# Kernel optimization log

Hardware: AMD Instinct MI355X
Metric: run time of the kernel (lower is better)

Reference implementation:

```python
import jax, jax.numpy as jnp
import numpy as np

B, T, H, DK = 4, 2048, 16, 64
F = H * DK
CK, NL = 64, 16  # chunk_size, num left chunks
MIN_VAL = float(np.finfo(np.float16).min)


def chunk_mask(size, ck, nl):
    # row i attends cols [max((i//ck - nl)*ck, 0), (i//ck + 1)*ck)
    i = jnp.arange(size)
    start = jnp.maximum((i // ck - nl) * ck, 0)
    end = (i // ck + 1) * ck
    j = jnp.arange(size)
    return (j[None, :] >= start[:, None]) & (j[None, :] < end[:, None])


def setup_inputs() -> dict:
    rng = jax.random.key(0)
    ks = jax.random.split(rng, 14)
    s = 1.0 / np.sqrt(F)
    mask = jnp.broadcast_to(chunk_mask(T, CK, NL)[None], (B, T, T))  # padding mask all-True & chunk band
    return {
        "query": jax.random.normal(ks[0], (B, T, F), jnp.float32),
        "key": jax.random.normal(ks[1], (B, T, F), jnp.float32),
        "value": jax.random.normal(ks[2], (B, T, F), jnp.float32),
        "pos_emb": jax.random.normal(ks[3], (1, T, F), jnp.float32),
        "mask": mask,
        "Wq": jax.random.normal(ks[4], (F, F), jnp.float32) * s,
        "bq": jnp.zeros((F,), jnp.float32),
        "Wk": jax.random.normal(ks[5], (F, F), jnp.float32) * s,
        "bk": jnp.zeros((F,), jnp.float32),
        "Wv": jax.random.normal(ks[6], (F, F), jnp.float32) * s,
        "bv": jnp.zeros((F,), jnp.float32),
        "Wp": jax.random.normal(ks[7], (F, F), jnp.float32) * s,
        "Wo": jax.random.normal(ks[8], (F, F), jnp.float32) * s,
        "bo": jnp.zeros((F,), jnp.float32),
        "pos_bias_u": jax.random.normal(ks[9], (H, DK), jnp.float32) * 0.05,
        "pos_bias_v": jax.random.normal(ks[10], (H, DK), jnp.float32) * 0.05,
    }


def reference(query, key, value, pos_emb, mask, Wq, bq, Wk, bk, Wv, bv, Wp, Wo, bo, pos_bias_u, pos_bias_v):
    b, t1, _ = query.shape
    t2 = key.shape[1]
    q = (query @ Wq.T + bq).reshape(b, t1, H, DK)            # (b, t1, h, d)
    k = (key @ Wk.T + bk).reshape(b, t2, H, DK).transpose(0, 2, 1, 3)   # (b, h, t2, d)
    v = (value @ Wv.T + bv).reshape(b, t2, H, DK).transpose(0, 2, 1, 3)  # (b, h, t2, d)
    p = (pos_emb @ Wp.T).reshape(pos_emb.shape[0], -1, H, DK).transpose(0, 2, 1, 3)[0]  # (h, t2, d)
    # matrix_ac: content score with bias u; matrix_bd: position score with bias v (no rel_shift in forward)
    matrix_ac = jnp.einsum('bthd,bhsd->bhts', q + pos_bias_u, k)
    matrix_bd = jnp.einsum('bthd,hsd->bhts', q + pos_bias_v, p)
    scores = (matrix_ac + matrix_bd) / np.sqrt(DK)
    m = mask[:, None, :, :]                                   # (b, 1, t1, t2)
    scores = jnp.where(m, scores, MIN_VAL)
    attn = jax.nn.softmax(scores, axis=-1)
    attn = jnp.where(m, attn, 0.0)
    x = jnp.einsum('bhts,bhsd->bthd', attn, v).reshape(b, t1, F)
    return x @ Wo.T + bo
```

## Files before the change

kernel.cpp:

```cpp
#include <hip/hip_runtime.h>
#include <hip/hip_bf16.h>

#define B_ 4
#define T_ 2048
#define H_ 16
#define DK_ 64
#define F_ 1024
#define SCALE_LOG2 0.18033688011112042f

typedef __bf16 bf16x8 __attribute__((ext_vector_type(8)));
typedef __bf16 bf16x4 __attribute__((ext_vector_type(4)));
typedef float f32x4 __attribute__((ext_vector_type(4)));

__device__ __forceinline__ void async_cp16(const void* g, void* l) {
  __builtin_amdgcn_global_load_lds((const __attribute__((address_space(1))) void*)g,
                                   (__attribute__((address_space(3))) void*)l, 16, 0, 0);
}

struct CvtArgs {
  const float* src[9];
  __bf16* dst[9];
  int n[9];
};
__global__ void cvt_all(CvtArgs a) {
  int t = blockIdx.y;
  int i = (blockIdx.x * 256 + threadIdx.x) * 8;
  if (i >= a.n[t]) return;
  const float* in = a.src[t];
  __bf16* out = a.dst[t];
  float4 x = *(const float4*)(in + i);
  float4 y = *(const float4*)(in + i + 4);
  bf16x8 o;
  o[0] = (__bf16)x.x; o[1] = (__bf16)x.y; o[2] = (__bf16)x.z; o[3] = (__bf16)x.w;
  o[4] = (__bf16)y.x; o[5] = (__bf16)y.y; o[6] = (__bf16)y.z; o[7] = (__bf16)y.w;
  *(bf16x8*)(out + i) = o;
}

struct GemmQKVP {
  const __bf16* W[4];
  const __bf16* Act[4];
  const float* bias[4];
  __bf16* out[4];
  int Nblocks[4];
};
__global__ __launch_bounds__(256) void gemm_qkvp(GemmQKVP g) {
  const int z = blockIdx.z;
  if ((int)blockIdx.x >= g.Nblocks[z]) return;
  const __bf16* __restrict__ A = g.W[z];
  const __bf16* __restrict__ Bm = g.Act[z];
  const float* __restrict__ bias = g.bias[z];
  __bf16* __restrict__ Cout = g.out[z];
  constexpr int K = F_;
  __shared__ __bf16 As[128 * 32];
  __shared__ __bf16 Bs[128 * 32];
  const int tid = threadIdx.x;
  const int wave = tid >> 6, lane = tid & 63;
  const int mrow = lane & 15, quad = lane >> 4;
  const long m0 = (long)blockIdx.y * 128;
  const long n0 = (long)blockIdx.x * 128;
  const int wr = (wave >> 1) * 64, wc = (wave & 1) * 64;
  const int srow = lane >> 2;
  const int scol = (lane & 3) * 8;
  f32x4 acc[4][4] = {};
  for (int k0 = 0; k0 < K; k0 += 32) {
    if (k0) __syncthreads();
    for (int ph = 0; ph < 2; ++ph) {
      int rb = ph * 64 + wave * 16;
      async_cp16(A + (m0 + rb + srow) * (long)K + k0 + scol, As + rb * 32);
      async_cp16(Bm + (n0 + rb + srow) * (long)K + k0 + scol, Bs + rb * 32);
    }
    __syncthreads();
    bf16x8 af[4], bf[4];
    for (int i = 0; i < 4; i++) af[i] = *(const bf16x8*)&As[(wr + i * 16 + mrow) * 32 + quad * 8];
    for (int j = 0; j < 4; j++) bf[j] = *(const bf16x8*)&Bs[(wc + j * 16 + mrow) * 32 + quad * 8];
    for (int i = 0; i < 4; i++)
      for (int j = 0; j < 4; j++)
        acc[i][j] = __builtin_amdgcn_mfma_f32_16x16x32_bf16(af[i], bf[j], acc[i][j], 0, 0, 0);
  }
  for (int i = 0; i < 4; i++) {
    int frow = (int)m0 + wr + i * 16 + quad * 4;
    float4 b4 = bias ? *(const float4*)&bias[frow] : make_float4(0.f, 0.f, 0.f, 0.f);
    int h = frow >> 6, dbase = frow & 63;
    for (int j = 0; j < 4; j++) {
      int token = (int)n0 + wc + j * 16 + mrow;
      int bb = token >> 11, tt = token & 2047;
      bf16x4 pk;
      pk[0] = (__bf16)(acc[i][j][0] + b4.x);
      pk[1] = (__bf16)(acc[i][j][1] + b4.y);
      pk[2] = (__bf16)(acc[i][j][2] + b4.z);
      pk[3] = (__bf16)(acc[i][j][3] + b4.w);
      *(bf16x4*)&Cout[(((long)(bb * H_ + h)) * T_ + tt) * DK_ + dbase] = pk;
    }
  }
}

__global__ __launch_bounds__(256) void gemm_out(
    const __bf16* __restrict__ A, const __bf16* __restrict__ Bm,
    float* __restrict__ Cout, const float* __restrict__ bias, int N, int K) {
  __shared__ __bf16 As[128 * 32];
  __shared__ __bf16 Bs[128 * 32];
  const int tid = threadIdx.x;
  const int wave = tid >> 6, lane = tid & 63;
  const int mrow = lane & 15, quad = lane >> 4;
  const long m0 = (long)blockIdx.y * 128, n0 = (long)blockIdx.x * 128;
  const int wr = (wave >> 1) * 64, wc = (wave & 1) * 64;
  const int srow = lane >> 2;
  const int scol = (lane & 3) * 8;
  f32x4 acc[4][4] = {};
  for (int k0 = 0; k0 < K; k0 += 32) {
    if (k0) __syncthreads();
    for (int ph = 0; ph < 2; ++ph) {
      int rb = ph * 64 + wave * 16;
      async_cp16(A + (m0 + rb + srow) * (long)K + k0 + scol, As + rb * 32);
      async_cp16(Bm + (n0 + rb + srow) * (long)K + k0 + scol, Bs + rb * 32);
    }
    __syncthreads();
    bf16x8 af[4], bf[4];
    for (int i = 0; i < 4; i++) af[i] = *(const bf16x8*)&As[(wr + i * 16 + mrow) * 32 + quad * 8];
    for (int j = 0; j < 4; j++) bf[j] = *(const bf16x8*)&Bs[(wc + j * 16 + mrow) * 32 + quad * 8];
    for (int i = 0; i < 4; i++)
      for (int j = 0; j < 4; j++)
        acc[i][j] = __builtin_amdgcn_mfma_f32_16x16x32_bf16(af[i], bf[j], acc[i][j], 0, 0, 0);
  }
  for (int i = 0; i < 4; i++) {
    int row = (int)m0 + wr + i * 16 + quad * 4;
    for (int j = 0; j < 4; j++) {
      int col = (int)n0 + wc + j * 16 + mrow;
      float bval = bias[col];
      for (int r = 0; r < 4; r++)
        Cout[(long)(row + r) * N + col] = acc[i][j][r] + bval;
    }
  }
}

__global__ __launch_bounds__(256) void prep(
    const __bf16* __restrict__ Ph, __bf16* __restrict__ Kh,
    const __bf16* __restrict__ Vh, __bf16* __restrict__ Vth,
    const float* __restrict__ u, const float* __restrict__ vb,
    float* __restrict__ biasC) {
  __shared__ __bf16 Vl[64 * 72];
  const int tc = blockIdx.x, h = blockIdx.y, b = blockIdx.z;
  const int tid = threadIdx.x;
  const int r4 = tid >> 2, c16 = (tid & 3) * 16;
  const long bh = b * H_ + h;
  const long kbase = (bh * T_ + tc * 64 + r4) * DK_ + c16;
  const long pbase = (((long)h) * T_ + tc * 64 + r4) * DK_ + c16;
  bf16x8 k0 = *(const bf16x8*)&Kh[kbase];
  bf16x8 k1 = *(const bf16x8*)&Kh[kbase + 8];
  bf16x8 p0 = *(const bf16x8*)&Ph[pbase];
  bf16x8 p1 = *(const bf16x8*)&Ph[pbase + 8];
  float4 u0 = *(const float4*)&u[h * 64 + c16];
  float4 u1 = *(const float4*)&u[h * 64 + c16 + 4];
  float4 u2 = *(const float4*)&u[h * 64 + c16 + 8];
  float4 u3 = *(const float4*)&u[h * 64 + c16 + 12];
  float4 v0 = *(const float4*)&vb[h * 64 + c16];
  float4 v1 = *(const float4*)&vb[h * 64 + c16 + 4];
  float4 v2 = *(const float4*)&vb[h * 64 + c16 + 8];
  float4 v3 = *(const float4*)&vb[h * 64 + c16 + 12];
  float s = 0.f;
  {
    const float uu[16] = {u0.x,u0.y,u0.z,u0.w,u1.x,u1.y,u1.z,u1.w,u2.x,u2.y,u2.z,u2.w,u3.x,u3.y,u3.z,u3.w};
    const float vv[16] = {v0.x,v0.y,v0.z,v0.w,v1.x,v1.y,v1.z,v1.w,v2.x,v2.y,v2.z,v2.w,v3.x,v3.y,v3.z,v3.w};
#pragma unroll
    for (int j = 0; j < 8; j++) {
      s += (float)k0[j] * uu[j] + (float)p0[j] * vv[j];
      s += (float)k1[j] * uu[8 + j] + (float)p1[j] * vv[8 + j];
    }
  }
  bf16x8 kp0, kp1;
#pragma unroll
  for (int j = 0; j < 8; j++) {
    kp0[j] = (__bf16)((float)k0[j] + (float)p0[j]);
    kp1[j] = (__bf16)((float)k1[j] + (float)p1[j]);
  }
  *(bf16x8*)&Kh[kbase] = kp0;
  *(bf16x8*)&Kh[kbase + 8] = kp1;
  s += __shfl_xor(s, 1);
  s += __shfl_xor(s, 2);
  if ((tid & 3) == 0) biasC[bh * T_ + tc * 64 + r4] = s * SCALE_LOG2;
  const long vbase = (bh * T_ + tc * 64 + r4) * DK_ + c16;
  bf16x8 vv0 = *(const bf16x8*)&Vh[vbase];
  bf16x8 vv1 = *(const bf16x8*)&Vh[vbase + 8];
  *(bf16x8*)&Vl[r4 * 72 + c16] = vv0;
  *(bf16x8*)&Vl[r4 * 72 + c16 + 8] = vv1;
  __syncthreads();
  const int d4 = tid >> 2, tcol = (tid & 3) * 16;
  bf16x8 o0, o1;
#pragma unroll
  for (int j = 0; j < 8; j++) {
    o0[j] = Vl[(tcol + j) * 72 + d4];
    o1[j] = Vl[(tcol + 8 + j) * 72 + d4];
  }
  long obase = (bh * DK_ + d4) * T_ + tc * 64 + tcol;
  *(bf16x8*)&Vth[obase] = o0;
  *(bf16x8*)&Vth[obase + 8] = o1;
}

template <int FULL>
__device__ __forceinline__ void attn_step2(
    int s0, long bh, int tid, int wave, int mrow, int quad,
    const __bf16* __restrict__ Kh, const __bf16* __restrict__ Vth,
    const float* __restrict__ Bp, const bf16x8 (&qf)[4][2],
    __bf16* Pl, __bf16* Vt, f32x4 accO[4], f32x4& accL) {
  __syncthreads();
  if (FULL) {
#pragma unroll
    for (int p = 0; p < 4; ++p) {
      int idx = tid + p * 256;
      int row = idx >> 4, colg = (idx & 15) * 8;
      *(bf16x8*)&Vt[row * 136 + colg] =
          *(const bf16x8*)&Vth[(bh * DK_ + row) * T_ + s0 + colg];
    }
  } else {
#pragma unroll
    for (int p = 0; p < 2; ++p) {
      int idx = tid + p * 256;
      int row = idx >> 3, colg = (idx & 7) * 8;
      *(bf16x8*)&Vt[row * 136 + colg] =
          *(const bf16x8*)&Vth[(bh * DK_ + row) * T_ + s0 + colg];
    }
  }
  if (FULL || wave < 2) {
    const int krow = s0 + wave * 32;
    bf16x8 kf[2][2];
#pragma unroll
    for (int nt = 0; nt < 2; ++nt)
#pragma unroll
      for (int kh = 0; kh < 2; ++kh)
        kf[nt][kh] = *(const bf16x8*)&Kh[(bh * T_ + krow + nt * 16 + mrow) * DK_ + kh * 32 + quad * 8];
    float bias01[2] = {Bp[krow + mrow], Bp[krow + 16 + mrow]};
    f32x4 s[4][2];
#pragma unroll
    for (int mt = 0; mt < 4; ++mt)
#pragma unroll
      for (int nt = 0; nt < 2; ++nt) {
        f32x4 a = {0.f, 0.f, 0.f, 0.f};
        a = __builtin_amdgcn_mfma_f32_16x16x32_bf16(qf[mt][0], kf[nt][0], a, 0, 0, 0);
        a = __builtin_amdgcn_mfma_f32_16x16x32_bf16(qf[mt][1], kf[nt][1], a, 0, 0, 0);
        s[mt][nt] = a;
      }
#pragma unroll
    for (int mt = 0; mt < 4; ++mt)
#pragma unroll
      for (int nt = 0; nt < 2; ++nt)
#pragma unroll
        for (int r = 0; r < 4; ++r) {
          float p = __builtin_amdgcn_exp2f(s[mt][nt][r] * SCALE_LOG2 + bias01[nt]);
          Pl[(mt * 16 + quad * 4 + r) * 136 + wave * 32 + nt * 16 + mrow] = (__bf16)p;
        }
  }
  __syncthreads();
  constexpr int NKT = FULL ? 4 : 2;
  bf16x8 ones;
#pragma unroll
  for (int j = 0; j < 8; ++j) ones[j] = (__bf16)1.0f;
  bf16x8 ap[NKT];
#pragma unroll
  for (int kt = 0; kt < NKT; ++kt)
    ap[kt] = *(const bf16x8*)&Pl[(wave * 16 + mrow) * 136 + kt * 32 + quad * 8];
#pragma unroll
  for (int kt = 0; kt < NKT; ++kt) {
    accL = __builtin_amdgcn_mfma_f32_16x16x32_bf16(ap[kt], ones, accL, 0, 0, 0);
#pragma unroll
    for (int nt = 0; nt < 4; ++nt) {
      bf16x8 bv = *(const bf16x8*)&Vt[(nt * 16 + mrow) * 136 + kt * 32 + quad * 8];
      accO[nt] = __builtin_amdgcn_mfma_f32_16x16x32_bf16(ap[kt], bv, accO[nt], 0, 0, 0);
    }
  }
}

__global__ __launch_bounds__(256) void attn_banded(
    const __bf16* __restrict__ Qh, const __bf16* __restrict__ Kh,
    const __bf16* __restrict__ Vth, const float* __restrict__ biasC,
    __bf16* __restrict__ X) {
  __shared__ __bf16 Pl[64 * 136];
  __shared__ __bf16 Vt[64 * 136];
  const int qc = blockIdx.x, h = blockIdx.y, b = blockIdx.z;
  const int tid = threadIdx.x, wave = tid >> 6, lane = tid & 63;
  const int mrow = lane & 15, quad = lane >> 4;
  const long bh = b * H_ + h;
  const int span = (qc >= 16 ? 17 : qc + 1);
  const int s_lo = (qc + 1 - span) * 64, s_hi = (qc + 1) * 64;
  const float* Bp = biasC + bh * T_;
  bf16x8 qf[4][2];
#pragma unroll
  for (int mt = 0; mt < 4; ++mt)
#pragma unroll
    for (int kh = 0; kh < 2; ++kh)
      qf[mt][kh] = *(const bf16x8*)&Qh[(bh * T_ + qc * 64 + mt * 16 + mrow) * DK_ + kh * 32 + quad * 8];
  f32x4 accO[4] = {};
  f32x4 accL = {0.f, 0.f, 0.f, 0.f};
  int s0 = s_lo;
  if (span & 1) {
    attn_step2<0>(s0, bh, tid, wave, mrow, quad, Kh, Vth, Bp, qf, Pl, Vt, accO, accL);
    s0 += 64;
  }
  for (; s0 < s_hi; s0 += 128)
    attn_step2<1>(s0, bh, tid, wave, mrow, quad, Kh, Vth, Bp, qf, Pl, Vt, accO, accL);
#pragma unroll
  for (int r = 0; r < 4; ++r) {
    float inv = 1.0f / accL[r];
    int t = qc * 64 + wave * 16 + quad * 4 + r;
#pragma unroll
    for (int nt = 0; nt < 4; ++nt)
      X[((long)(b * T_ + t) * H_ + h) * DK_ + nt * 16 + mrow] = (__bf16)(accO[nt][r] * inv);
  }
}

extern "C" void kernel_launch(void* const* d_in, const int* in_sizes, int n_in,
                              void* d_out, int out_size, void* d_ws, size_t ws_size,
                              hipStream_t stream) {
  (void)in_sizes; (void)n_in; (void)out_size; (void)ws_size;
  const float* query = (const float*)d_in[0];
  const float* key   = (const float*)d_in[1];
  const float* value = (const float*)d_in[2];
  const float* pos   = (const float*)d_in[3];
  const float* Wq = (const float*)d_in[5];
  const float* bq = (const float*)d_in[6];
  const float* Wk = (const float*)d_in[7];
  const float* bk = (const float*)d_in[8];
  const float* Wv = (const float*)d_in[9];
  const float* bv = (const float*)d_in[10];
  const float* Wp = (const float*)d_in[11];
  const float* Wo = (const float*)d_in[12];
  const float* bo = (const float*)d_in[13];
  const float* pu = (const float*)d_in[14];
  const float* pvb = (const float*)d_in[15];

  const long NQ = (long)B_ * T_ * F_;
  const long NP = (long)T_ * F_;
  const long NW = (long)F_ * F_;
  char* ws = (char*)d_ws;
  __bf16* qb  = (__bf16*)ws; ws += NQ * 2;
  __bf16* kb  = (__bf16*)ws; ws += NQ * 2;
  __bf16* vbm = (__bf16*)ws; ws += NQ * 2;
  __bf16* pb  = (__bf16*)ws; ws += NP * 2;
  __bf16* wqb = (__bf16*)ws; ws += NW * 2;
  __bf16* wkb = (__bf16*)ws; ws += NW * 2;
  __bf16* wvb = (__bf16*)ws; ws += NW * 2;
  __bf16* wpb = (__bf16*)ws; ws += NW * 2;
  __bf16* wob = (__bf16*)ws; ws += NW * 2;
  __bf16* Qh  = (__bf16*)ws; ws += NQ * 2;
  __bf16* Kh  = (__bf16*)ws; ws += NQ * 2;
  __bf16* Vh  = (__bf16*)ws; ws += NQ * 2;
  __bf16* Ph  = (__bf16*)ws; ws += NP * 2;
  float*  biasC = (float*)ws; ws += (long)B_ * H_ * T_ * 4;
  __bf16* Vth = kb;
  __bf16* Xb  = qb;

  {
    CvtArgs ca;
    ca.src[0] = query; ca.dst[0] = qb;  ca.n[0] = (int)NQ;
    ca.src[1] = key;   ca.dst[1] = kb;  ca.n[1] = (int)NQ;
    ca.src[2] = value; ca.dst[2] = vbm; ca.n[2] = (int)NQ;
    ca.src[3] = pos;   ca.dst[3] = pb;  ca.n[3] = (int)NP;
    ca.src[4] = Wq;    ca.dst[4] = wqb; ca.n[4] = (int)NW;
    ca.src[5] = Wk;    ca.dst[5] = wkb; ca.n[5] = (int)NW;
    ca.src[6] = Wv;    ca.dst[6] = wvb; ca.n[6] = (int)NW;
    ca.src[7] = Wp;    ca.dst[7] = wpb; ca.n[7] = (int)NW;
    ca.src[8] = Wo;    ca.dst[8] = wob; ca.n[8] = (int)NW;
    cvt_all<<<dim3(4096, 9), 256, 0, stream>>>(ca);
  }
  {
    GemmQKVP g;
    g.W[0] = wqb; g.Act[0] = qb;  g.bias[0] = bq;      g.out[0] = Qh; g.Nblocks[0] = 64;
    g.W[1] = wkb; g.Act[1] = kb;  g.bias[1] = bk;      g.out[1] = Kh; g.Nblocks[1] = 64;
    g.W[2] = wvb; g.Act[2] = vbm; g.bias[2] = bv;      g.out[2] = Vh; g.Nblocks[2] = 64;
    g.W[3] = wpb; g.Act[3] = pb;  g.bias[3] = nullptr; g.out[3] = Ph; g.Nblocks[3] = 16;
    gemm_qkvp<<<dim3(64, 8, 4), 256, 0, stream>>>(g);
  }
  prep<<<dim3(32, 16, 4), 256, 0, stream>>>(Ph, Kh, Vh, Vth, pu, pvb, biasC);
  attn_banded<<<dim3(32, 16, 4), 256, 0, stream>>>(Qh, Kh, Vth, biasC, Xb);
  gemm_out<<<dim3(8, 64), 256, 0, stream>>>(Xb, wob, (float*)d_out, bo, F_, F_);
}
```

Before: 421.3 us.

## Rewrite QKVP projection GEMM as 256x256 double-buffered 8-wave pipelined kernel

Replaces the 128x128, 4-wave QKVP projection GEMM with a 256x256 tile, 512-thread kernel. It uses a 128KB double-buffered LDS ring with XOR-swizzled layout and asynchronous global-to-LDS loads interleaved between four MFMA phases, managed with explicit vmcnt waits, barriers and setprio. The goal is to hide global latency, avoid LDS bank conflicts and raise arithmetic intensity per loaded byte. The cost is fewer blocks (512 total) and heavy register and LDS use, so occupancy and tail effects could hurt, especially for the small P projection.

Result: faster. 404.0 us (-4.1%).

```diff
diff --git a/kernel.cpp b/kernel.cpp
--- a/kernel.cpp
+++ b/kernel.cpp
@@ -36,60 +36,153 @@
   *(bf16x8*)(out + i) = o;
 }
 
-struct GemmQKVP {
-  const __bf16* W[4];
-  const __bf16* Act[4];
+struct G8 {
+  const __bf16* A[4];
+  const __bf16* Bm[4];
   const float* bias[4];
   __bf16* out[4];
-  int Nblocks[4];
+  int nx[4];
 };
-__global__ __launch_bounds__(256) void gemm_qkvp(GemmQKVP g) {
+
+__global__ __launch_bounds__(512, 2) void gemm_qkvp8(G8 g) {
   const int z = blockIdx.z;
-  if ((int)blockIdx.x >= g.Nblocks[z]) return;
-  const __bf16* __restrict__ A = g.W[z];
-  const __bf16* __restrict__ Bm = g.Act[z];
+  if ((int)blockIdx.x >= g.nx[z]) return;
+  constexpr int K = F_;
+  constexpr int NT = K / 64;
+  __shared__ __bf16 LDS[65536];
+  const __bf16* __restrict__ A = g.A[z];
+  const __bf16* __restrict__ Bmm = g.Bm[z];
   const float* __restrict__ bias = g.bias[z];
-  __bf16* __restrict__ Cout = g.out[z];
-  constexpr int K = F_;
-  __shared__ __bf16 As[128 * 32];
-  __shared__ __bf16 Bs[128 * 32];
+  __bf16* __restrict__ Co = g.out[z];
   const int tid = threadIdx.x;
   const int wave = tid >> 6, lane = tid & 63;
   const int mrow = lane & 15, quad = lane >> 4;
-  const long m0 = (long)blockIdx.y * 128;
-  const long n0 = (long)blockIdx.x * 128;
-  const int wr = (wave >> 1) * 64, wc = (wave & 1) * 64;
-  const int srow = lane >> 2;
-  const int scol = (lane & 3) * 8;
-  f32x4 acc[4][4] = {};
-  for (int k0 = 0; k0 < K; k0 += 32) {
-    if (k0) __syncthreads();
-    for (int ph = 0; ph < 2; ++ph) {
-      int rb = ph * 64 + wave * 16;
-      async_cp16(A + (m0 + rb + srow) * (long)K + k0 + scol, As + rb * 32);
-      async_cp16(Bm + (n0 + rb + srow) * (long)K + k0 + scol, Bs + rb * 32);
-    }
-    __syncthreads();
-    bf16x8 af[4], bf[4];
-    for (int i = 0; i < 4; i++) af[i] = *(const bf16x8*)&As[(wr + i * 16 + mrow) * 32 + quad * 8];
-    for (int j = 0; j < 4; j++) bf[j] = *(const bf16x8*)&Bs[(wc + j * 16 + mrow) * 32 + quad * 8];
-    for (int i = 0; i < 4; i++)
-      for (int j = 0; j < 4; j++)
-        acc[i][j] = __builtin_amdgcn_mfma_f32_16x16x32_bf16(af[i], bf[j], acc[i][j], 0, 0, 0);
-  }
-  for (int i = 0; i < 4; i++) {
-    int frow = (int)m0 + wr + i * 16 + quad * 4;
+  const int wm = wave >> 2, wn = wave & 3;
+  const long m0 = (long)blockIdx.y * 256;
+  const long n0 = (long)blockIdx.x * 256;
+  const int srow = tid >> 3;
+  const int sslot = tid & 7;
+  const int scol = ((sslot ^ (srow & 7)) * 8);
+  const __bf16* sA = A + (m0 + srow) * K + scol;
+  const __bf16* sB = Bmm + (n0 + srow) * K + scol;
+  const int ldsw = wave * 512;
+  const int csw0 = ((quad) ^ (mrow & 7)) * 8;
+  const int csw1 = ((4 + quad) ^ (mrow & 7)) * 8;
+
+#define STAGE_A(t_, h_)                                              \
+  do {                                                               \
+    __bf16* lb_ = &LDS[(((t_)&1) * 2 + (h_)) * 8192 + ldsw];         \
+    const __bf16* ga_ = sA + (h_) * (128 * K) + (t_)*64;             \
+    async_cp16(ga_, lb_);                                            \
+    async_cp16(ga_ + 64 * K, lb_ + 4096);                            \
+  } while (0)
+#define STAGE_B(t_, h_)                                              \
+  do {                                                               \
+    __bf16* lb_ = &LDS[32768 + (((t_)&1) * 2 + (h_)) * 8192 + ldsw]; \
+    const __bf16* gb_ = sB + (h_) * (128 * K) + (t_)*64;             \
+    async_cp16(gb_, lb_);                                            \
+    async_cp16(gb_ + 64 * K, lb_ + 4096);                            \
+  } while (0)
+
+  f32x4 acc[8][4] = {};
+  bf16x8 af[8][2], bf[4][2];
+  STAGE_A(0, 0); STAGE_A(0, 1); STAGE_B(0, 0); STAGE_B(0, 1);
+  STAGE_A(1, 0); STAGE_A(1, 1);
+
+#pragma unroll 2
+  for (int t = 0; t < NT; ++t) {
+    const int d = t & 1;
+    const __bf16* Ab = &LDS[(d * 2 + wm) * 8192];
+    const __bf16* Bb = &LDS[32768 + (d * 2 + (wn >> 1)) * 8192 + (wn & 1) * 4096];
+    if (t + 1 < NT) {
+      STAGE_B(t + 1, 0);
+      asm volatile("s_waitcnt vmcnt(6)" ::: "memory");
+    } else {
+      asm volatile("s_waitcnt vmcnt(0)" ::: "memory");
+    }
+    __builtin_amdgcn_s_barrier();
+#pragma unroll
+    for (int fr = 0; fr < 4; ++fr) {
+      af[fr][0] = *(const bf16x8*)&Ab[(fr * 16 + mrow) * 64 + csw0];
+      af[fr][1] = *(const bf16x8*)&Ab[(fr * 16 + mrow) * 64 + csw1];
+    }
+#pragma unroll
+    for (int fc = 0; fc < 2; ++fc) {
+      bf[fc][0] = *(const bf16x8*)&Bb[(fc * 16 + mrow) * 64 + csw0];
+      bf[fc][1] = *(const bf16x8*)&Bb[(fc * 16 + mrow) * 64 + csw1];
+    }
+    __builtin_amdgcn_s_setprio(1);
+#pragma unroll
+    for (int fr = 0; fr < 4; ++fr)
+#pragma unroll
+      for (int fc = 0; fc < 2; ++fc) {
+        acc[fr][fc] = __builtin_amdgcn_mfma_f32_16x16x32_bf16(af[fr][0], bf[fc][0], acc[fr][fc], 0, 0, 0);
+        acc[fr][fc] = __builtin_amdgcn_mfma_f32_16x16x32_bf16(af[fr][1], bf[fc][1], acc[fr][fc], 0, 0, 0);
+      }
+    __builtin_amdgcn_s_setprio(0);
+    __builtin_amdgcn_s_barrier();
+    if (t + 1 < NT) STAGE_B(t + 1, 1);
+#pragma unroll
+    for (int fr = 4; fr < 8; ++fr) {
+      af[fr][0] = *(const bf16x8*)&Ab[(fr * 16 + mrow) * 64 + csw0];
+      af[fr][1] = *(const bf16x8*)&Ab[(fr * 16 + mrow) * 64 + csw1];
+    }
+#pragma unroll
+    for (int fc = 2; fc < 4; ++fc) {
+      bf[fc][0] = *(const bf16x8*)&Bb[(fc * 16 + mrow) * 64 + csw0];
+      bf[fc][1] = *(const bf16x8*)&Bb[(fc * 16 + mrow) * 64 + csw1];
+    }
+    __builtin_amdgcn_s_setprio(1);
+#pragma unroll
+    for (int fr = 4; fr < 8; ++fr)
+#pragma unroll
+      for (int fc = 2; fc < 4; ++fc) {
+        acc[fr][fc] = __builtin_amdgcn_mfma_f32_16x16x32_bf16(af[fr][0], bf[fc][0], acc[fr][fc], 0, 0, 0);
+        acc[fr][fc] = __builtin_amdgcn_mfma_f32_16x16x32_bf16(af[fr][1], bf[fc][1], acc[fr][fc], 0, 0, 0);
+      }
+    __builtin_amdgcn_s_setprio(0);
+    __builtin_amdgcn_s_barrier();
+    if (t + 2 < NT) STAGE_A(t + 2, 0);
+    __builtin_amdgcn_s_setprio(1);
+#pragma unroll
+    for (int fr = 0; fr < 4; ++fr)
+#pragma unroll
+      for (int fc = 2; fc < 4; ++fc) {
+        acc[fr][fc] = __builtin_amdgcn_mfma_f32_16x16x32_bf16(af[fr][0], bf[fc][0], acc[fr][fc], 0, 0, 0);
+        acc[fr][fc] = __builtin_amdgcn_mfma_f32_16x16x32_bf16(af[fr][1], bf[fc][1], acc[fr][fc], 0, 0, 0);
+      }
+    __builtin_amdgcn_s_setprio(0);
+    __builtin_amdgcn_s_barrier();
+    if (t + 2 < NT) STAGE_A(t + 2, 1);
+    __builtin_amdgcn_s_setprio(1);
+#pragma unroll
+    for (int fr = 4; fr < 8; ++fr)
+#pragma unroll
+      for (int fc = 0; fc < 2; ++fc) {
+        acc[fr][fc] = __builtin_amdgcn_mfma_f32_16x16x32_bf16(af[fr][0], bf[fc][0], acc[fr][fc], 0, 0, 0);
+        acc[fr][fc] = __builtin_amdgcn_mfma_f32_16x16x32_bf16(af[fr][1], bf[fc][1], acc[fr][fc], 0, 0, 0);
+      }
+    __builtin_amdgcn_s_setprio(0);
+    __builtin_amdgcn_s_barrier();
+  }
+#undef STAGE_A
+#undef STAGE_B
+
+#pragma unroll
+  for (int fr = 0; fr < 8; ++fr) {
+    int frow = (int)m0 + wm * 128 + fr * 16 + quad * 4;
     float4 b4 = bias ? *(const float4*)&bias[frow] : make_float4(0.f, 0.f, 0.f, 0.f);
     int h = frow >> 6, dbase = frow & 63;
-    for (int j = 0; j < 4; j++) {
-      int token = (int)n0 + wc + j * 16 + mrow;
+#pragma unroll
+    for (int fc = 0; fc < 4; ++fc) {
+      int token = (int)n0 + wn * 64 + fc * 16 + mrow;
       int bb = token >> 11, tt = token & 2047;
       bf16x4 pk;
-      pk[0] = (__bf16)(acc[i][j][0] + b4.x);
-      pk[1] = (__bf16)(acc[i][j][1] + b4.y);
-      pk[2] = (__bf16)(acc[i][j][2] + b4.z);
-      pk[3] = (__bf16)(acc[i][j][3] + b4.w);
-      *(bf16x4*)&Cout[(((long)(bb * H_ + h)) * T_ + tt) * DK_ + dbase] = pk;
+      pk[0] = (__bf16)(acc[fr][fc][0] + b4.x);
+      pk[1] = (__bf16)(acc[fr][fc][1] + b4.y);
+      pk[2] = (__bf16)(acc[fr][fc][2] + b4.z);
+      pk[3] = (__bf16)(acc[fr][fc][3] + b4.w);
+      *(bf16x4*)&Co[(((long)(bb * H_ + h)) * T_ + tt) * DK_ + dbase] = pk;
     }
   }
 }
@@ -362,12 +455,12 @@
     cvt_all<<<dim3(4096, 9), 256, 0, stream>>>(ca);
   }
   {
-    GemmQKVP g;
-    g.W[0] = wqb; g.Act[0] = qb;  g.bias[0] = bq;      g.out[0] = Qh; g.Nblocks[0] = 64;
-    g.W[1] = wkb; g.Act[1] = kb;  g.bias[1] = bk;      g.out[1] = Kh; g.Nblocks[1] = 64;
-    g.W[2] = wvb; g.Act[2] = vbm; g.bias[2] = bv;      g.out[2] = Vh; g.Nblocks[2] = 64;
-    g.W[3] = wpb; g.Act[3] = pb;  g.bias[3] = nullptr; g.out[3] = Ph; g.Nblocks[3] = 16;
-    gemm_qkvp<<<dim3(64, 8, 4), 256, 0, stream>>>(g);
+    G8 g;
+    g.A[0] = wqb; g.Bm[0] = qb;  g.bias[0] = bq;      g.out[0] = Qh; g.nx[0] = 32;
+    g.A[1] = wkb; g.Bm[1] = kb;  g.bias[1] = bk;      g.out[1] = Kh; g.nx[1] = 32;
+    g.A[2] = wvb; g.Bm[2] = vbm; g.bias[2] = bv;      g.out[2] = Vh; g.nx[2] = 32;
+    g.A[3] = wpb; g.Bm[3] = pb;  g.bias[3] = nullptr; g.out[3] = Ph; g.nx[3] = 8;
+    gemm_qkvp8<<<dim3(32, 4, 4), 512, 0, stream>>>(g);
   }
   prep<<<dim3(32, 16, 4), 256, 0, stream>>>(Ph, Kh, Vh, Vth, pu, pvb, biasC);
   attn_banded<<<dim3(32, 16, 4), 256, 0, stream>>>(Qh, Kh, Vth, biasC, Xb);
```
